# Kernel tuning notes

Hardware: AMD Instinct MI355X
Metric: run time of the kernel (lower is better)

The kernel has to match this reference:

```python
import jax, jax.numpy as jnp
import numpy as np

MAX_EVENTS = 100  # decoder steps (undefined global in source)

def _make_pe(seq_len, d):
    pos = jnp.arange(seq_len, dtype=jnp.float32)[:, None]
    div = jnp.exp(jnp.arange(0, d, 2, dtype=jnp.float32) * (-np.log(10000.0) / d))
    pe = jnp.zeros((seq_len, d), dtype=jnp.float32)
    pe = pe.at[:, 0::2].set(jnp.sin(pos * div))
    pe = pe.at[:, 1::2].set(jnp.cos(pos * div))
    return pe

def _gru_combine(gi, gh, h):
    # PyTorch GRU gate order: r, z, n
    ir, iz, inn = jnp.split(gi, 3, axis=-1)
    hr, hz, hn = jnp.split(gh, 3, axis=-1)
    r = jax.nn.sigmoid(ir + hr)
    z = jax.nn.sigmoid(iz + hz)
    n = jnp.tanh(inn + r * hn)
    return (1.0 - z) * n + z * h

def setup_inputs() -> dict:
    key = jax.random.key(0)
    d = 768
    bs, seq = 64, 300
    ks = jax.random.split(key, 18)
    s = 0.02
    return {
        'x': jax.random.normal(ks[0], (bs, seq, d), jnp.float32),
        'enc_Wih': jax.random.normal(ks[1], (3 * d, d), jnp.float32) * s,
        'enc_Whh': jax.random.normal(ks[2], (3 * d, d), jnp.float32) * s,
        'enc_bih': jax.random.normal(ks[3], (3 * d,), jnp.float32) * s,
        'enc_bhh': jax.random.normal(ks[4], (3 * d,), jnp.float32) * s,
        'dec_Wih': jax.random.normal(ks[5], (3 * d, 1 + d), jnp.float32) * s,
        'dec_Whh': jax.random.normal(ks[6], (3 * d, d), jnp.float32) * s,
        'dec_bih': jax.random.normal(ks[7], (3 * d,), jnp.float32) * s,
        'dec_bhh': jax.random.normal(ks[8], (3 * d,), jnp.float32) * s,
        'qW': jax.random.normal(ks[9], (d, d), jnp.float32) * s,
        'qb': jax.random.normal(ks[10], (d,), jnp.float32) * s,
        'mW': jax.random.normal(ks[11], (d, d), jnp.float32) * s,
        'mb': jax.random.normal(ks[12], (d,), jnp.float32) * s,
        'pW': jax.random.normal(ks[13], (1, d), jnp.float32) * s,
        'pb': jax.random.normal(ks[14], (1,), jnp.float32) * s,
        'tW': jax.random.normal(ks[15], (1, d), jnp.float32) * s,
        'tb': jax.random.normal(ks[16], (1,), jnp.float32) * s,
    }

def reference(x, enc_Wih, enc_Whh, enc_bih, enc_bhh,
              dec_Wih, dec_Whh, dec_bih, dec_bhh,
              qW, qb, mW, mb, pW, pb, tW, tb):
    bs, seq, d = x.shape
    # positional encoding (dropout in eval mode -> identity)
    x = x + _make_pe(seq, d)[None, :, :]

    # encoder GRU: precompute input projections, scan over time
    gi_all = jnp.einsum('bsd,gd->sbg', x, enc_Wih) + enc_bih  # (seq, bs, 3d)
    h0 = jnp.zeros((bs, d), x.dtype)

    def enc_step(h, gi):
        gh = h @ enc_Whh.T + enc_bhh
        h_new = _gru_combine(gi, gh, h)
        return h_new, h_new

    _, enc_seq = jax.lax.scan(enc_step, h0, gi_all)
    enc_outputs = jnp.transpose(enc_seq, (1, 0, 2))  # (bs, seq, d)

    # memory projection (loop-invariant; same math as recomputing each step)
    mem = jnp.einsum('bsd,ed->bse', enc_outputs, mW) + mb  # (bs, seq, d)

    def dec_step(carry, _):
        h, last = carry  # h: (bs, d), last: (bs, 1)
        q = h @ qW.T + qb  # (bs, d)
        logits = jnp.tanh(mem + q[:, None, :]) @ pW[0] + pb[0]  # (bs, seq)
        w = jax.nn.softmax(logits, axis=1)
        ctx = jnp.einsum('bs,bsd->bd', w, enc_outputs)
        xin = jnp.concatenate([last, ctx], axis=-1)  # (bs, 1+d)
        gi = xin @ dec_Wih.T + dec_bih
        gh = h @ dec_Whh.T + dec_bhh
        h_new = _gru_combine(gi, gh, h)
        pred = h_new @ tW.T + tb  # (bs, 1)
        return (h_new, pred), pred

    last0 = jnp.zeros((bs, 1), x.dtype)
    _, preds = jax.lax.scan(dec_step, (h0, last0), None, length=MAX_EVENTS)
    return jnp.transpose(preds, (1, 0, 2))  # (bs, MAX_EVENTS, 1)
```

## Files before the change

### kernel.cpp

```cpp
#include <hip/hip_runtime.h>
#include <hip/hip_bf16.h>
#include <cstdint>
#include <cstddef>

#define D    768
#define G3   2304
#define BS   64
#define SEQ  300
#define TDEC 100
#define TCH  25
#define NCH  12
#define NBLK 512
#define NH   (D * 64)

#define BAR_GRP(g)  ((g) * 32)
#define BAR_TOP     512
#define BAR_GEN0    544
#define BAR_GENL(g) (576 + (g) * 32)
#define BAR_SIZE    2048

typedef unsigned int u32;
typedef unsigned long long u64;

__device__ __forceinline__ float sigf(float x) { return 1.0f / (1.0f + __expf(-x)); }
__device__ __forceinline__ float tanhfast(float x) {
    float e = __expf(2.0f * x);
    return 1.0f - 2.0f / (e + 1.0f);
}
__device__ __forceinline__ void bf2x(u32 u, float& a, float& b) {
    union { u32 i; float f; } xx, yy;
    xx.i = u << 16; yy.i = u & 0xffff0000u; a = xx.f; b = yy.f;
}

#define DOT4(acc, wv, x0, x1, x2, x3) \
    acc = fmaf((wv).x,(x0), fmaf((wv).y,(x1), fmaf((wv).z,(x2), fmaf((wv).w,(x3),(acc)))))

__device__ __forceinline__ void stG(float* p, float v) {
    __hip_atomic_store(p, v, __ATOMIC_RELAXED, __HIP_MEMORY_SCOPE_AGENT);
}
__device__ __forceinline__ void stG64(u64* p, u64 v) {
    __hip_atomic_store(p, v, __ATOMIC_RELAXED, __HIP_MEMORY_SCOPE_AGENT);
}
__device__ __forceinline__ float ldGf(const float* p) {
    return __hip_atomic_load(p, __ATOMIC_RELAXED, __HIP_MEMORY_SCOPE_AGENT);
}
__device__ __forceinline__ u32 ldGu(const u32* p) {
    return __hip_atomic_load(p, __ATOMIC_RELAXED, __HIP_MEMORY_SCOPE_AGENT);
}
__device__ __forceinline__ u32 f2bfu(float f) {
    __hip_bfloat16 h = __float2bfloat16(f);
    unsigned short s; __builtin_memcpy(&s, &h, 2); return (u32)s;
}
__device__ __forceinline__ float bfsel(u32 w, int sh) {
    union { u32 i; float f; } u; u.i = ((w >> sh) & 0xffffu) << 16; return u.f;
}

__device__ __forceinline__ void gridbar(u32* B, u32 idx) {
    __builtin_amdgcn_fence(__ATOMIC_RELEASE, "workgroup");
    __syncthreads();
    if (threadIdx.x == 0) {
        const u32 g = blockIdx.x >> 5;
        u32 old = __hip_atomic_fetch_add(&B[BAR_GRP(g)], 1u, __ATOMIC_RELAXED, __HIP_MEMORY_SCOPE_AGENT);
        if (old == idx * 32u - 1u) {
            u32 o2 = __hip_atomic_fetch_add(&B[BAR_TOP], 1u, __ATOMIC_RELAXED, __HIP_MEMORY_SCOPE_AGENT);
            if (o2 == idx * 16u - 1u) {
                __hip_atomic_store(&B[BAR_GEN0], idx, __ATOMIC_RELAXED, __HIP_MEMORY_SCOPE_AGENT);
            } else {
                while (__hip_atomic_load(&B[BAR_GEN0], __ATOMIC_RELAXED, __HIP_MEMORY_SCOPE_AGENT) < idx)
                    __builtin_amdgcn_s_sleep(4);
            }
            __hip_atomic_store(&B[BAR_GENL(g)], idx, __ATOMIC_RELAXED, __HIP_MEMORY_SCOPE_AGENT);
        } else {
            while (__hip_atomic_load(&B[BAR_GENL(g)], __ATOMIC_RELAXED, __HIP_MEMORY_SCOPE_AGENT) < idx)
                __builtin_amdgcn_s_sleep(8);
        }
    }
    __syncthreads();
}

__global__ __launch_bounds__(256) void kPrep(
    const float* __restrict__ decWih,
    float* __restrict__ Wc, float* __restrict__ W0,
    float* __restrict__ hSeq0, float* __restrict__ hDs0,
    float* __restrict__ lastP, u32* __restrict__ barW)
{
    const int NW = G3 * 769;
    const int NB = 2 * BAR_SIZE;
    const int TOT = NW + 2 * NH + 64 + NB;
    const int stride = gridDim.x * blockDim.x;
    for (int u = blockIdx.x * blockDim.x + threadIdx.x; u < TOT; u += stride) {
        if (u < NW) {
            int g = u / 769; int c = u % 769;
            float w = decWih[u];
            if (c == 0) W0[g] = w; else Wc[(size_t)g * D + (c - 1)] = w;
        } else if (u < NW + NH) {
            hSeq0[u - NW] = 0.0f;
        } else if (u < NW + 2 * NH) {
            hDs0[u - NW - NH] = 0.0f;
        } else if (u < NW + 2 * NH + 64) {
            lastP[u - NW - 2 * NH] = 0.0f;
        } else {
            barW[u - NW - 2 * NH - 64] = 0;
        }
    }
}

__device__ __forceinline__ void gi_tile(
    const float* __restrict__ x, const float* __restrict__ Wih,
    __hip_bfloat16* __restrict__ giB, float* __restrict__ As, float* __restrict__ Bs,
    int m0, int tc, int t)
{
    const int tid = threadIdx.x;
    const int lr = tid >> 2;
    const int lk = (tid & 3) * 4;
    const int tm = (tid >> 4) * 4;
    const int tn = (tid & 15) * 4;
    const float tf = (float)t;

    float acc[4][4];
    #pragma unroll
    for (int i = 0; i < 4; ++i)
        #pragma unroll
        for (int j = 0; j < 4; ++j) acc[i][j] = 0.f;

    for (int kc = 0; kc < D; kc += 16) {
        const float4 a4 = *(const float4*)(Wih + (size_t)(m0 + lr) * D + kc + lk);
        float4 b4 = *(const float4*)(x + ((size_t)lr * SEQ + t) * D + kc + lk);
        const int i0 = (kc + lk) >> 1;
        const float dv0 = __expf(-0.0239852614f * (float)i0);
        const float dv1 = __expf(-0.0239852614f * (float)(i0 + 1));
        float s0, c0, s1, c1;
        __sincosf(tf * dv0, &s0, &c0);
        __sincosf(tf * dv1, &s1, &c1);
        b4.x += s0; b4.y += c0; b4.z += s1; b4.w += c1;
        As[(lk + 0) * 64 + lr] = a4.x; As[(lk + 1) * 64 + lr] = a4.y;
        As[(lk + 2) * 64 + lr] = a4.z; As[(lk + 3) * 64 + lr] = a4.w;
        Bs[(lk + 0) * 64 + lr] = b4.x; Bs[(lk + 1) * 64 + lr] = b4.y;
        Bs[(lk + 2) * 64 + lr] = b4.z; Bs[(lk + 3) * 64 + lr] = b4.w;
        __syncthreads();
        #pragma unroll
        for (int k = 0; k < 16; ++k) {
            const float4 av = *(const float4*)(As + k * 64 + tm);
            const float4 bv = *(const float4*)(Bs + k * 64 + tn);
            acc[0][0] = fmaf(av.x, bv.x, acc[0][0]); acc[0][1] = fmaf(av.x, bv.y, acc[0][1]);
            acc[0][2] = fmaf(av.x, bv.z, acc[0][2]); acc[0][3] = fmaf(av.x, bv.w, acc[0][3]);
            acc[1][0] = fmaf(av.y, bv.x, acc[1][0]); acc[1][1] = fmaf(av.y, bv.y, acc[1][1]);
            acc[1][2] = fmaf(av.y, bv.z, acc[1][2]); acc[1][3] = fmaf(av.y, bv.w, acc[1][3]);
            acc[2][0] = fmaf(av.z, bv.x, acc[2][0]); acc[2][1] = fmaf(av.z, bv.y, acc[2][1]);
            acc[2][2] = fmaf(av.z, bv.z, acc[2][2]); acc[2][3] = fmaf(av.z, bv.w, acc[2][3]);
            acc[3][0] = fmaf(av.w, bv.x, acc[3][0]); acc[3][1] = fmaf(av.w, bv.y, acc[3][1]);
            acc[3][2] = fmaf(av.w, bv.z, acc[3][2]); acc[3][3] = fmaf(av.w, bv.w, acc[3][3]);
        }
        __syncthreads();
    }
    #pragma unroll
    for (int i = 0; i < 4; ++i) {
        u32 lo = f2bfu(acc[i][0]) | (f2bfu(acc[i][1]) << 16);
        u32 hi = f2bfu(acc[i][2]) | (f2bfu(acc[i][3]) << 16);
        u64 v = ((u64)hi << 32) | (u64)lo;
        stG64((u64*)(giB + ((size_t)tc * G3 + m0 + tm + i) * 64 + tn), v);
    }
}

__device__ __forceinline__ void enc_step(
    const __hip_bfloat16* __restrict__ giT, const float* __restrict__ Whh,
    const float* __restrict__ bih, const float* __restrict__ bhh,
    const float* __restrict__ hrd, float* __restrict__ hwr,
    __hip_bfloat16* __restrict__ encB, int t, float* __restrict__ lds_h)
{
    const int tid = threadIdx.x;
    const int b   = tid & 63;
    const int jw  = __builtin_amdgcn_readfirstlane((int)(blockIdx.x * 4 + (tid >> 6)));

    const float* whr = Whh + (size_t)jw * D;
    const float* whz = Whh + (size_t)(768 + jw) * D;
    const float* whn = Whh + (size_t)(1536 + jw) * D;

    float ahr = 0.f, ahz = 0.f, ahn = 0.f;
    for (int kc = 0; kc < D; kc += 64) {
        const float4* gh = (const float4*)(hrd + kc * 64);
        float4* lh = (float4*)lds_h;
        #pragma unroll
        for (int it = 0; it < 4; ++it) lh[tid + 256 * it] = gh[tid + 256 * it];
        __syncthreads();
        #pragma unroll
        for (int kk = 0; kk < 64; kk += 4) {
            const float4 v3 = *(const float4*)(whr + kc + kk);
            const float4 v4 = *(const float4*)(whz + kc + kk);
            const float4 v5 = *(const float4*)(whn + kc + kk);
            const float h0 = lds_h[(kk + 0) * 64 + b];
            const float h1 = lds_h[(kk + 1) * 64 + b];
            const float h2 = lds_h[(kk + 2) * 64 + b];
            const float h3 = lds_h[(kk + 3) * 64 + b];
            DOT4(ahr, v3, h0, h1, h2, h3);
            DOT4(ahz, v4, h0, h1, h2, h3);
            DOT4(ahn, v5, h0, h1, h2, h3);
        }
        __syncthreads();
    }
    const u32* gp = (const u32*)giT;
    const int bo = b >> 1, sh = (b & 1) << 4;
    const u32 w0 = ldGu(gp + (size_t)jw * 32 + bo);
    const u32 w1 = ldGu(gp + (size_t)(768 + jw) * 32 + bo);
    const u32 w2 = ldGu(gp + (size_t)(1536 + jw) * 32 + bo);
    const float gir = bfsel(w0, sh);
    const float giz = bfsel(w1, sh);
    const float gin = bfsel(w2, sh);
    const float r = sigf(gir + bih[jw] + ahr + bhh[jw]);
    const float z = sigf(giz + bih[768 + jw] + ahz + bhh[768 + jw]);
    const float n = tanhfast(gin + bih[1536 + jw] + r * (ahn + bhh[1536 + jw]));
    const float ho = hrd[jw * 64 + b];
    const float hn = (1.f - z) * n + z * ho;
    stG(hwr + jw * 64 + b, hn);
    encB[((size_t)b * SEQ + t) * D + jw] = __float2bfloat16(hn);
}

__global__ __launch_bounds__(256) void kEncPersist(
    const float* __restrict__ x, const float* __restrict__ eWih,
    const float* __restrict__ eWhh, const float* __restrict__ ebih,
    const float* __restrict__ ebhh, __hip_bfloat16* __restrict__ giB,
    float* __restrict__ hSeq, __hip_bfloat16* __restrict__ encB, u32* bar)
{
    __shared__ float smem[4096];
    u32 bars = 0;
    for (int c = 0; c < NCH; ++c) {
        for (int job = blockIdx.x; job < 36 * TCH; job += NBLK)
            gi_tile(x, eWih, giB, smem, smem + 1024,
                    (job % 36) * 64, job / 36, c * TCH + job / 36);
        gridbar(bar, ++bars);
        for (int tc = 0; tc < TCH; ++tc) {
            const int t = c * TCH + tc;
            if (blockIdx.x < 192)
                enc_step(giB + (size_t)tc * G3 * 64, eWhh, ebih, ebhh,
                         hSeq + (size_t)t * NH, hSeq + (size_t)(t + 1) * NH, encB, t, smem);
            gridbar(bar, ++bars);
        }
    }
}

__global__ __launch_bounds__(256) void kGemmMem(
    const __hip_bfloat16* __restrict__ encB, const float* __restrict__ mW,
    const float* __restrict__ mb, __hip_bfloat16* __restrict__ memB)
{
    __shared__ float As[16 * 64];
    __shared__ float Bs[16 * 64];
    const int tid = threadIdx.x;
    const int m0 = blockIdx.y * 64, n0 = blockIdx.x * 64;
    const int lr = tid >> 2;
    const int lk = (tid & 3) * 4;
    const int tm = (tid >> 4) * 4;
    const int tn = (tid & 15) * 4;

    float acc[4][4];
    #pragma unroll
    for (int i = 0; i < 4; ++i)
        #pragma unroll
        for (int j = 0; j < 4; ++j) acc[i][j] = 0.f;

    for (int kc = 0; kc < D; kc += 16) {
        const uint2 ua = *(const uint2*)(encB + (size_t)(m0 + lr) * D + kc + lk);
        float a0, a1, a2, a3;
        bf2x(ua.x, a0, a1); bf2x(ua.y, a2, a3);
        const float4 b4 = *(const float4*)(mW + (size_t)(n0 + lr) * D + kc + lk);
        As[(lk + 0) * 64 + lr] = a0; As[(lk + 1) * 64 + lr] = a1;
        As[(lk + 2) * 64 + lr] = a2; As[(lk + 3) * 64 + lr] = a3;
        Bs[(lk + 0) * 64 + lr] = b4.x; Bs[(lk + 1) * 64 + lr] = b4.y;
        Bs[(lk + 2) * 64 + lr] = b4.z; Bs[(lk + 3) * 64 + lr] = b4.w;
        __syncthreads();
        #pragma unroll
        for (int k = 0; k < 16; ++k) {
            const float4 av = *(const float4*)(As + k * 64 + tm);
            const float4 bv = *(const float4*)(Bs + k * 64 + tn);
            acc[0][0] = fmaf(av.x, bv.x, acc[0][0]); acc[0][1] = fmaf(av.x, bv.y, acc[0][1]);
            acc[0][2] = fmaf(av.x, bv.z, acc[0][2]); acc[0][3] = fmaf(av.x, bv.w, acc[0][3]);
            acc[1][0] = fmaf(av.y, bv.x, acc[1][0]); acc[1][1] = fmaf(av.y, bv.y, acc[1][1]);
            acc[1][2] = fmaf(av.y, bv.z, acc[1][2]); acc[1][3] = fmaf(av.y, bv.w, acc[1][3]);
            acc[2][0] = fmaf(av.z, bv.x, acc[2][0]); acc[2][1] = fmaf(av.z, bv.y, acc[2][1]);
            acc[2][2] = fmaf(av.z, bv.z, acc[2][2]); acc[2][3] = fmaf(av.z, bv.w, acc[2][3]);
            acc[3][0] = fmaf(av.w, bv.x, acc[3][0]); acc[3][1] = fmaf(av.w, bv.y, acc[3][1]);
            acc[3][2] = fmaf(av.w, bv.z, acc[3][2]); acc[3][3] = fmaf(av.w, bv.w, acc[3][3]);
        }
        __syncthreads();
    }
    const float bb0 = mb[n0 + tn + 0], bb1 = mb[n0 + tn + 1];
    const float bb2 = mb[n0 + tn + 2], bb3 = mb[n0 + tn + 3];
    #pragma unroll
    for (int i = 0; i < 4; ++i) {
        __hip_bfloat16* row = memB + (size_t)(m0 + tm + i) * D + n0 + tn;
        row[0] = __float2bfloat16(acc[i][0] + bb0);
        row[1] = __float2bfloat16(acc[i][1] + bb1);
        row[2] = __float2bfloat16(acc[i][2] + bb2);
        row[3] = __float2bfloat16(acc[i][3] + bb3);
    }
}

__device__ __forceinline__ void dec_q(
    const float* __restrict__ qW, const float* __restrict__ qb,
    const float* __restrict__ hrd, float* __restrict__ qTt,
    float* __restrict__ lds_h, float* __restrict__ lds_t)
{
    const int tid = threadIdx.x;
    const int b   = tid & 63;
    const int wv  = tid >> 6;
    const int jw  = __builtin_amdgcn_readfirstlane((int)(blockIdx.x * 4 + wv));
    const float* w = qW + (size_t)jw * D;
    float acc = 0.f;
    for (int kc = 0; kc < D; kc += 64) {
        const float4* gh = (const float4*)(hrd + kc * 64);
        float4* lh = (float4*)lds_h;
        #pragma unroll
        for (int it = 0; it < 4; ++it) lh[tid + 256 * it] = gh[tid + 256 * it];
        __syncthreads();
        #pragma unroll
        for (int kk = 0; kk < 64; kk += 4) {
            const float4 w4 = *(const float4*)(w + kc + kk);
            acc = fmaf(w4.x, lds_h[(kk + 0) * 64 + b], acc);
            acc = fmaf(w4.y, lds_h[(kk + 1) * 64 + b], acc);
            acc = fmaf(w4.z, lds_h[(kk + 2) * 64 + b], acc);
            acc = fmaf(w4.w, lds_h[(kk + 3) * 64 + b], acc);
        }
        __syncthreads();
    }
    lds_t[b * 4 + wv] = acc + qb[jw];
    __syncthreads();
    if (tid < 128) {
        const int bb = tid >> 1, hf = (tid & 1) * 2;
        float2 v; v.x = lds_t[bb * 4 + hf]; v.y = lds_t[bb * 4 + hf + 1];
        u64 uv; __builtin_memcpy(&uv, &v, 8);
        stG64((u64*)(qTt + (size_t)bb * D + blockIdx.x * 4 + hf), uv);
    }
}

__device__ __forceinline__ void dec_attn(
    const float* __restrict__ qTt, const __hip_bfloat16* __restrict__ memB,
    const __hip_bfloat16* __restrict__ encB, const float* __restrict__ pW,
    const float* __restrict__ pb, float* __restrict__ ctxP, float* __restrict__ seP,
    float* __restrict__ sm)
{
    const int tid = threadIdx.x;
    const int b  = blockIdx.x & 63;
    const int ch = blockIdx.x >> 6;
    float* s_q  = sm;
    float* s_pw = sm + 768;
    float* s_cx = sm + 1536;
    float* s_se = sm + 2304;
    for (int i = tid; i < 768; i += 256) {
        s_q[i]  = qTt[(size_t)b * D + i];
        s_pw[i] = pW[i];
        s_cx[i] = 0.f;
    }
    if (tid == 0) s_se[0] = 0.f;
    __syncthreads();
    const int lane = tid & 63;
    const int wv   = tid >> 6;
    const int d0_0 = lane * 4, d0_1 = 256 + lane * 4, d0_2 = 512 + lane * 4;
    const float4 qv0 = *(const float4*)(s_q + d0_0);
    const float4 qv1 = *(const float4*)(s_q + d0_1);
    const float4 qv2 = *(const float4*)(s_q + d0_2);
    const float4 pv0 = *(const float4*)(s_pw + d0_0);
    const float4 pv1 = *(const float4*)(s_pw + d0_1);
    const float4 pv2 = *(const float4*)(s_pw + d0_2);
    float cacc[12];
    #pragma unroll
    for (int i = 0; i < 12; ++i) cacc[i] = 0.f;
    float seacc = 0.f;
    const float pbv = pb[0];
    const size_t rowb = (size_t)b * SEQ;
    int s = ch + 8 * wv;
    uint2 mu0, mu1, mu2, eu0, eu1, eu2;
    if (s < SEQ) {
        const __hip_bfloat16* mrow = memB + (rowb + s) * D;
        const __hip_bfloat16* erow = encB + (rowb + s) * D;
        mu0 = *(const uint2*)(mrow + d0_0); mu1 = *(const uint2*)(mrow + d0_1); mu2 = *(const uint2*)(mrow + d0_2);
        eu0 = *(const uint2*)(erow + d0_0); eu1 = *(const uint2*)(erow + d0_1); eu2 = *(const uint2*)(erow + d0_2);
    }
    while (s < SEQ) {
        const int sn = s + 32;
        const bool pf = sn < SEQ;
        uint2 nm0, nm1, nm2, ne0, ne1, ne2;
        if (pf) {
            const __hip_bfloat16* mrow = memB + (rowb + sn) * D;
            const __hip_bfloat16* erow = encB + (rowb + sn) * D;
            nm0 = *(const uint2*)(mrow + d0_0); nm1 = *(const uint2*)(mrow + d0_1); nm2 = *(const uint2*)(mrow + d0_2);
            ne0 = *(const uint2*)(erow + d0_0); ne1 = *(const uint2*)(erow + d0_1); ne2 = *(const uint2*)(erow + d0_2);
        }
        float lp = 0.f;
        float m0, m1, m2, m3;
        bf2x(mu0.x, m0, m1); bf2x(mu0.y, m2, m3);
        lp = fmaf(pv0.x, tanhfast(m0 + qv0.x), lp);
        lp = fmaf(pv0.y, tanhfast(m1 + qv0.y), lp);
        lp = fmaf(pv0.z, tanhfast(m2 + qv0.z), lp);
        lp = fmaf(pv0.w, tanhfast(m3 + qv0.w), lp);
        bf2x(mu1.x, m0, m1); bf2x(mu1.y, m2, m3);
        lp = fmaf(pv1.x, tanhfast(m0 + qv1.x), lp);
        lp = fmaf(pv1.y, tanhfast(m1 + qv1.y), lp);
        lp = fmaf(pv1.z, tanhfast(m2 + qv1.z), lp);
        lp = fmaf(pv1.w, tanhfast(m3 + qv1.w), lp);
        bf2x(mu2.x, m0, m1); bf2x(mu2.y, m2, m3);
        lp = fmaf(pv2.x, tanhfast(m0 + qv2.x), lp);
        lp = fmaf(pv2.y, tanhfast(m1 + qv2.y), lp);
        lp = fmaf(pv2.z, tanhfast(m2 + qv2.z), lp);
        lp = fmaf(pv2.w, tanhfast(m3 + qv2.w), lp);
        #pragma unroll
        for (int o = 32; o > 0; o >>= 1) lp += __shfl_xor(lp, o, 64);
        const float e = __expf(lp + pbv);
        seacc += e;
        float e0, e1, e2, e3;
        bf2x(eu0.x, e0, e1); bf2x(eu0.y, e2, e3);
        cacc[0] = fmaf(e, e0, cacc[0]); cacc[1] = fmaf(e, e1, cacc[1]);
        cacc[2] = fmaf(e, e2, cacc[2]); cacc[3] = fmaf(e, e3, cacc[3]);
        bf2x(eu1.x, e0, e1); bf2x(eu1.y, e2, e3);
        cacc[4] = fmaf(e, e0, cacc[4]); cacc[5] = fmaf(e, e1, cacc[5]);
        cacc[6] = fmaf(e, e2, cacc[6]); cacc[7] = fmaf(e, e3, cacc[7]);
        bf2x(eu2.x, e0, e1); bf2x(eu2.y, e2, e3);
        cacc[8]  = fmaf(e, e0, cacc[8]);  cacc[9]  = fmaf(e, e1, cacc[9]);
        cacc[10] = fmaf(e, e2, cacc[10]); cacc[11] = fmaf(e, e3, cacc[11]);
        if (pf) { mu0 = nm0; mu1 = nm1; mu2 = nm2; eu0 = ne0; eu1 = ne1; eu2 = ne2; }
        s = sn;
    }
    #pragma unroll
    for (int g = 0; g < 3; ++g) {
        const int d0 = g * 256 + lane * 4;
        atomicAdd(&s_cx[d0 + 0], cacc[g * 4 + 0]);
        atomicAdd(&s_cx[d0 + 1], cacc[g * 4 + 1]);
        atomicAdd(&s_cx[d0 + 2], cacc[g * 4 + 2]);
        atomicAdd(&s_cx[d0 + 3], cacc[g * 4 + 3]);
    }
    if (lane == 0) atomicAdd(&s_se[0], seacc);
    __syncthreads();
    float* crow = ctxP + (size_t)(ch * 64 + b) * D;
    for (int i = tid; i < 768; i += 256) stG(crow + i, s_cx[i]);
    if (tid == 0) stG(seP + ch * 64 + b, s_se[0]);
}

__device__ __forceinline__ void dec_combine(
    const float* __restrict__ ctxP, const float* __restrict__ seP,
    float* __restrict__ ctxCt, float* __restrict__ seCt)
{
    const int b = blockIdx.x;
    const int tid = threadIdx.x;
    for (int i = tid; i < 768; i += 256) {
        float s = 0.f;
        #pragma unroll
        for (int ch = 0; ch < 8; ++ch)
            s += ldGf(ctxP + (size_t)(ch * 64 + b) * D + i);
        stG(ctxCt + (size_t)b * D + i, s);
    }
    if (tid == 0) {
        float s = 0.f;
        #pragma unroll
        for (int ch = 0; ch < 8; ++ch) s += ldGf(seP + ch * 64 + b);
        stG(seCt + b, s);
    }
}

__device__ __forceinline__ void dec_reduce(
    const float* __restrict__ ppt, const float* __restrict__ tb,
    float* __restrict__ lastN, float* __restrict__ out, int t, float* __restrict__ sm)
{
    const int b = blockIdx.x - 448;
    const int tid = threadIdx.x;
    float v = 0.f;
    if (tid < 192) v = ppt[(size_t)b * 192 + tid];
    #pragma unroll
    for (int o = 32; o > 0; o >>= 1) v += __shfl_xor(v, o, 64);
    if ((tid & 63) == 0) sm[tid >> 6] = v;
    __syncthreads();
    if (tid == 0) {
        const float p = sm[0] + sm[1] + sm[2] + sm[3] + tb[0];
        out[(size_t)b * TDEC + t] = p;
        stG(lastN + b, p);
    }
    __syncthreads();
}

__device__ __forceinline__ void dec_cell(
    const float* __restrict__ Wc, const float* __restrict__ W0,
    const float* __restrict__ dWhh, const float* __restrict__ dbih,
    const float* __restrict__ dbhh, const float* __restrict__ tW,
    const float* __restrict__ ctxFt, const float* __restrict__ seFt,
    const float* __restrict__ lastT, float* __restrict__ ppt,
    const float* __restrict__ hrd, float* __restrict__ hwr,
    float* __restrict__ lds_h, float* __restrict__ lds_c)
{
    const int tid = threadIdx.x;
    const int b   = tid & 63;
    const int q4  = tid >> 6;
    const int jw  = __builtin_amdgcn_readfirstlane((int)(blockIdx.x * 4 + q4));
    const float* whr = dWhh + (size_t)jw * D;
    const float* whz = dWhh + (size_t)(768 + jw) * D;
    const float* whn = dWhh + (size_t)(1536 + jw) * D;
    const float* wcr = Wc + (size_t)jw * D;
    const float* wcz = Wc + (size_t)(768 + jw) * D;
    const float* wcn = Wc + (size_t)(1536 + jw) * D;
    float cir = 0.f, ciz = 0.f, cin_ = 0.f, ahr = 0.f, ahz = 0.f, ahn = 0.f;
    for (int kc = 0; kc < D; kc += 64) {
        const float4* gh = (const float4*)(hrd + kc * 64);
        float4* lh = (float4*)lds_h;
        #pragma unroll
        for (int it = 0; it < 4; ++it) lh[tid + 256 * it] = gh[tid + 256 * it];
        {
            const float4* cp = (const float4*)(ctxFt + (size_t)b * D + kc + q4 * 16);
            const float4 c0 = cp[0], c1 = cp[1], c2 = cp[2], c3 = cp[3];
            const int k0 = q4 * 16;
            lds_c[(k0 +  0) * 64 + b] = c0.x; lds_c[(k0 +  1) * 64 + b] = c0.y;
            lds_c[(k0 +  2) * 64 + b] = c0.z; lds_c[(k0 +  3) * 64 + b] = c0.w;
            lds_c[(k0 +  4) * 64 + b] = c1.x; lds_c[(k0 +  5) * 64 + b] = c1.y;
            lds_c[(k0 +  6) * 64 + b] = c1.z; lds_c[(k0 +  7) * 64 + b] = c1.w;
            lds_c[(k0 +  8) * 64 + b] = c2.x; lds_c[(k0 +  9) * 64 + b] = c2.y;
            lds_c[(k0 + 10) * 64 + b] = c2.z; lds_c[(k0 + 11) * 64 + b] = c2.w;
            lds_c[(k0 + 12) * 64 + b] = c3.x; lds_c[(k0 + 13) * 64 + b] = c3.y;
            lds_c[(k0 + 14) * 64 + b] = c3.z; lds_c[(k0 + 15) * 64 + b] = c3.w;
        }
        __syncthreads();
        #pragma unroll
        for (int kk = 0; kk < 64; kk += 4) {
            const float4 v0 = *(const float4*)(wcr + kc + kk);
            const float4 v1 = *(const float4*)(wcz + kc + kk);
            const float4 v2 = *(const float4*)(wcn + kc + kk);
            const float4 v3 = *(const float4*)(whr + kc + kk);
            const float4 v4 = *(const float4*)(whz + kc + kk);
            const float4 v5 = *(const float4*)(whn + kc + kk);
            const float c0 = lds_c[(kk + 0) * 64 + b];
            const float c1 = lds_c[(kk + 1) * 64 + b];
            const float c2 = lds_c[(kk + 2) * 64 + b];
            const float c3 = lds_c[(kk + 3) * 64 + b];
            const float h0 = lds_h[(kk + 0) * 64 + b];
            const float h1 = lds_h[(kk + 1) * 64 + b];
            const float h2 = lds_h[(kk + 2) * 64 + b];
            const float h3 = lds_h[(kk + 3) * 64 + b];
            DOT4(cir, v0, c0, c1, c2, c3);
            DOT4(ciz, v1, c0, c1, c2, c3);
            DOT4(cin_, v2, c0, c1, c2, c3);
            DOT4(ahr, v3, h0, h1, h2, h3);
            DOT4(ahz, v4, h0, h1, h2, h3);
            DOT4(ahn, v5, h0, h1, h2, h3);
        }
        __syncthreads();
    }
    const float inv = 1.f / seFt[b];
    const float lst = lastT[b];
    const float gir = cir * inv + W0[jw] * lst + dbih[jw];
    const float giz = ciz * inv + W0[768 + jw] * lst + dbih[768 + jw];
    const float gin = cin_ * inv + W0[1536 + jw] * lst + dbih[1536 + jw];
    const float r = sigf(gir + ahr + dbhh[jw]);
    const float z = sigf(giz + ahz + dbhh[768 + jw]);
    const float n = tanhfast(gin + r * (ahn + dbhh[1536 + jw]));
    const float ho = hrd[jw * 64 + b];
    const float hn = (1.f - z) * n + z * ho;
    stG(hwr + jw * 64 + b, hn);

    __syncthreads();
    lds_h[q4 * 64 + b] = tW[jw] * hn;
    __syncthreads();
    if (tid < 64) {
        const float p = lds_h[tid] + lds_h[64 + tid] + lds_h[128 + tid] + lds_h[192 + tid];
        stG(ppt + (size_t)tid * 192 + blockIdx.x, p);
    }
}

__global__ __launch_bounds__(256) void kDecPersist(
    const float* __restrict__ Wc, const float* __restrict__ W0,
    const float* __restrict__ dWhh, const float* __restrict__ dbih,
    const float* __restrict__ dbhh, const float* __restrict__ tW,
    const float* __restrict__ tb, const float* __restrict__ qW,
    const float* __restrict__ qb,
    const __hip_bfloat16* __restrict__ memB, const __hip_bfloat16* __restrict__ encB,
    const float* __restrict__ pW, const float* __restrict__ pb,
    float* __restrict__ qTu, float* __restrict__ ctxP, float* __restrict__ seP,
    float* __restrict__ ctxC, float* __restrict__ seC,
    float* __restrict__ predP, float* __restrict__ lastP,
    float* __restrict__ hDs, float* __restrict__ out, u32* bar)
{
    __shared__ float smem[8192];
    u32 bars = 0;
    for (int t = 0; t < TDEC; ++t) {
        const float* hr = hDs + (size_t)t * NH;
        float*       hw = hDs + (size_t)(t + 1) * NH;
        if (blockIdx.x < 192)
            dec_q(qW, qb, hr, qTu + (size_t)t * BS * D, smem, smem + 4096);
        else if (blockIdx.x >= 448 && t > 0)
            dec_reduce(predP + (size_t)(t - 1) * 64 * 192, tb,
                       lastP + (size_t)t * 64, out, t - 1, smem);
        gridbar(bar, ++bars);
        dec_attn(qTu + (size_t)t * BS * D, memB, encB, pW, pb, ctxP, seP, smem);
        gridbar(bar, ++bars);
        if (blockIdx.x < 64)
            dec_combine(ctxP, seP, ctxC + (size_t)t * BS * D, seC + (size_t)t * 64);
        gridbar(bar, ++bars);
        if (blockIdx.x < 192)
            dec_cell(Wc, W0, dWhh, dbih, dbhh, tW,
                     ctxC + (size_t)t * BS * D, seC + (size_t)t * 64,
                     lastP + (size_t)t * 64, predP + (size_t)t * 64 * 192,
                     hr, hw, smem, smem + 4096);
        gridbar(bar, ++bars);
    }
    if (blockIdx.x >= 448)
        dec_reduce(predP + (size_t)(TDEC - 1) * 64 * 192, tb,
                   lastP + (size_t)TDEC * 64, out, TDEC - 1, smem);
}

extern "C" void kernel_launch(void* const* d_in, const int* in_sizes, int n_in,
                              void* d_out, int out_size, void* d_ws, size_t ws_size,
                              hipStream_t stream) {
    const float* x    = (const float*)d_in[0];
    const float* eWih = (const float*)d_in[1];
    const float* eWhh = (const float*)d_in[2];
    const float* ebih = (const float*)d_in[3];
    const float* ebhh = (const float*)d_in[4];
    const float* dWih = (const float*)d_in[5];
    const float* dWhh = (const float*)d_in[6];
    const float* dbih = (const float*)d_in[7];
    const float* dbhh = (const float*)d_in[8];
    const float* qW   = (const float*)d_in[9];
    const float* qb   = (const float*)d_in[10];
    const float* mW   = (const float*)d_in[11];
    const float* mb   = (const float*)d_in[12];
    const float* pW   = (const float*)d_in[13];
    const float* pb   = (const float*)d_in[14];
    const float* tW   = (const float*)d_in[15];
    const float* tb   = (const float*)d_in[16];
    float* out = (float*)d_out;

    char* w = (char*)d_ws;
    auto alloc = [&](size_t bytes) -> char* {
        char* p = w; w += (bytes + 255) & ~(size_t)255; return p;
    };
    float* Wc    = (float*)alloc((size_t)G3 * D * 4);
    float* W0    = (float*)alloc((size_t)G3 * 4);
    __hip_bfloat16* encB = (__hip_bfloat16*)alloc((size_t)BS * SEQ * D * 2);
    __hip_bfloat16* memB = (__hip_bfloat16*)alloc((size_t)BS * SEQ * D * 2);
    __hip_bfloat16* giB  = (__hip_bfloat16*)alloc((size_t)TCH * G3 * 64 * 2);
    float* hSeq  = (float*)alloc((size_t)(SEQ + 1) * NH * 4);
    float* hDs   = (float*)alloc((size_t)(TDEC + 1) * NH * 4);
    float* qTu   = (float*)alloc((size_t)TDEC * BS * D * 4);
    float* ctxP  = (float*)alloc((size_t)8 * BS * D * 4);
    float* seP   = (float*)alloc(8 * 64 * 4);
    float* ctxC  = (float*)alloc((size_t)TDEC * BS * D * 4);
    float* seC   = (float*)alloc((size_t)TDEC * 64 * 4);
    float* predP = (float*)alloc((size_t)TDEC * 64 * 192 * 4);
    float* lastP = (float*)alloc((size_t)(TDEC + 1) * 64 * 4);
    u32*   barW  = (u32*)alloc((size_t)2 * BAR_SIZE * 4);

    kPrep<<<512, 256, 0, stream>>>(dWih, Wc, W0, hSeq, hDs, lastP, barW);
    kEncPersist<<<NBLK, 256, 0, stream>>>(x, eWih, eWhh, ebih, ebhh, giB, hSeq, encB, barW);
    kGemmMem<<<dim3(12, 300), 256, 0, stream>>>(encB, mW, mb, memB);
    kDecPersist<<<NBLK, 256, 0, stream>>>(Wc, W0, dWhh, dbih, dbhh, tW, tb, qW, qb,
                                          memB, encB, pW, pb, qTu, ctxP, seP, ctxC, seC,
                                          predP, lastP, hDs, out, barW + BAR_SIZE);
}
```

Baseline: 23.30 ms.

## Add XCD-local fast grid barriers and overlap encoder input GEMM with recurrence

New measurement: 22.26 ms. 4.4% less time.

```diff
diff --git a/kernel.cpp b/kernel.cpp
--- a/kernel.cpp
+++ b/kernel.cpp
@@ -13,11 +13,21 @@
 #define NBLK 512
 #define NH   (D * 64)
 
-#define BAR_GRP(g)  ((g) * 32)
-#define BAR_TOP     512
-#define BAR_GEN0    544
-#define BAR_GENL(g) (576 + (g) * 32)
-#define BAR_SIZE    2048
+#define R_SLOW_GRP(g)  ((g) * 32)
+#define R_SLOW_TOP     512
+#define R_SLOW_GEN0    544
+#define R_SLOW_GENL(g) (576 + (g) * 32)
+#define R_FA_LARR      1088
+#define R_FA_GENL      1344
+#define R_FA_TOP       1600
+#define R_FA_GEN0      1632
+#define R_FB_LARR      1664
+#define R_FB_GENL      1920
+#define R_FB_TOP       2176
+#define R_FB_GEN0      2208
+#define R_PROBE(g)     (2240 + (g) * 32)
+#define R_VOTE         2496
+#define R_SIZE         4096
 
 typedef unsigned int u32;
 typedef unsigned long long u64;
@@ -55,27 +65,80 @@
     union { u32 i; float f; } u; u.i = ((w >> sh) & 0xffffu) << 16; return u.f;
 }
 
-__device__ __forceinline__ void gridbar(u32* B, u32 idx) {
+__device__ __forceinline__ u32 add_wg(u32* p, u32 v) {
+    return __hip_atomic_fetch_add(p, v, __ATOMIC_RELAXED, __HIP_MEMORY_SCOPE_WORKGROUP);
+}
+__device__ __forceinline__ u32 add_ag(u32* p, u32 v) {
+    return __hip_atomic_fetch_add(p, v, __ATOMIC_RELAXED, __HIP_MEMORY_SCOPE_AGENT);
+}
+__device__ __forceinline__ void st_ag(u32* p, u32 v) {
+    __hip_atomic_store(p, v, __ATOMIC_RELAXED, __HIP_MEMORY_SCOPE_AGENT);
+}
+__device__ __forceinline__ u32 ld_ag(const u32* p) {
+    return __hip_atomic_load(p, __ATOMIC_RELAXED, __HIP_MEMORY_SCOPE_AGENT);
+}
+
+__device__ __forceinline__ uint2 ldnt2(const __hip_bfloat16* p) {
+    u64 v = __builtin_nontemporal_load((const u64*)p);
+    uint2 r; r.x = (u32)v; r.y = (u32)(v >> 32); return r;
+}
+
+__device__ __forceinline__ void bar_slow(u32* B, u32 idx) {
     __builtin_amdgcn_fence(__ATOMIC_RELEASE, "workgroup");
     __syncthreads();
     if (threadIdx.x == 0) {
         const u32 g = blockIdx.x >> 5;
-        u32 old = __hip_atomic_fetch_add(&B[BAR_GRP(g)], 1u, __ATOMIC_RELAXED, __HIP_MEMORY_SCOPE_AGENT);
+        u32 old = add_ag(&B[R_SLOW_GRP(g)], 1u);
         if (old == idx * 32u - 1u) {
-            u32 o2 = __hip_atomic_fetch_add(&B[BAR_TOP], 1u, __ATOMIC_RELAXED, __HIP_MEMORY_SCOPE_AGENT);
+            u32 o2 = add_ag(&B[R_SLOW_TOP], 1u);
             if (o2 == idx * 16u - 1u) {
-                __hip_atomic_store(&B[BAR_GEN0], idx, __ATOMIC_RELAXED, __HIP_MEMORY_SCOPE_AGENT);
+                st_ag(&B[R_SLOW_GEN0], idx);
             } else {
-                while (__hip_atomic_load(&B[BAR_GEN0], __ATOMIC_RELAXED, __HIP_MEMORY_SCOPE_AGENT) < idx)
-                    __builtin_amdgcn_s_sleep(4);
+                while (ld_ag(&B[R_SLOW_GEN0]) < idx) __builtin_amdgcn_s_sleep(4);
             }
-            __hip_atomic_store(&B[BAR_GENL(g)], idx, __ATOMIC_RELAXED, __HIP_MEMORY_SCOPE_AGENT);
+            st_ag(&B[R_SLOW_GENL(g)], idx);
         } else {
-            while (__hip_atomic_load(&B[BAR_GENL(g)], __ATOMIC_RELAXED, __HIP_MEMORY_SCOPE_AGENT) < idx)
-                __builtin_amdgcn_s_sleep(8);
-        }
-    }
-    __syncthreads();
+            while (ld_ag(&B[R_SLOW_GENL(g)]) < idx) __builtin_amdgcn_s_sleep(8);
+        }
+    }
+    __syncthreads();
+}
+
+__device__ __forceinline__ void bar_fast(u32* R, int larr, int genl, int top, int gen0,
+                                         u32 idx, u32 perClass) {
+    __builtin_amdgcn_fence(__ATOMIC_RELEASE, "workgroup");
+    __syncthreads();
+    if (threadIdx.x == 0) {
+        const int g = blockIdx.x & 7;
+        u32 old = add_wg(&R[larr + g * 32], 1u);
+        if (old == idx * perClass - 1u) {
+            u32 o2 = add_ag(&R[top], 1u);
+            if (o2 == idx * 8u - 1u) {
+                st_ag(&R[gen0], idx);
+            } else {
+                while (ld_ag(&R[gen0]) < idx) __builtin_amdgcn_s_sleep(2);
+            }
+            st_ag(&R[genl + g * 32], idx);
+        } else {
+            while (ld_ag(&R[genl + g * 32]) < idx) __builtin_amdgcn_s_sleep(4);
+        }
+    }
+    __syncthreads();
+}
+#define BAR_FA(R, i, n) bar_fast((R), R_FA_LARR, R_FA_GENL, R_FA_TOP, R_FA_GEN0, (i), (n))
+#define BAR_FB(R, i, n) bar_fast((R), R_FB_LARR, R_FB_GENL, R_FB_TOP, R_FB_GEN0, (i), (n))
+
+__device__ __forceinline__ u32 censusRun(u32* R, u32* sflag) {
+    if (threadIdx.x == 0) add_wg(&R[R_PROBE(blockIdx.x & 7)], 1u);
+    bar_slow(R, 1);
+    if (threadIdx.x == 0) {
+        u32 old = add_wg(&R[R_PROBE(blockIdx.x & 7)], 1u);
+        add_ag(&R[R_VOTE], (old >= (u32)(NBLK / 8)) ? 1u : 0u);
+    }
+    bar_slow(R, 2);
+    if (threadIdx.x == 0) *sflag = (ld_ag(&R[R_VOTE]) == (u32)NBLK) ? 1u : 0u;
+    __syncthreads();
+    return *sflag;
 }
 
 __global__ __launch_bounds__(256) void kPrep(
@@ -85,7 +148,7 @@
     float* __restrict__ lastP, u32* __restrict__ barW)
 {
     const int NW = G3 * 769;
-    const int NB = 2 * BAR_SIZE;
+    const int NB = 2 * R_SIZE;
     const int TOT = NW + 2 * NH + 64 + NB;
     const int stride = gridDim.x * blockDim.x;
     for (int u = blockIdx.x * blockDim.x + threadIdx.x; u < TOT; u += stride) {
@@ -219,21 +282,50 @@
     const float* __restrict__ x, const float* __restrict__ eWih,
     const float* __restrict__ eWhh, const float* __restrict__ ebih,
     const float* __restrict__ ebhh, __hip_bfloat16* __restrict__ giB,
-    float* __restrict__ hSeq, __hip_bfloat16* __restrict__ encB, u32* bar)
+    float* __restrict__ hSeq, __hip_bfloat16* __restrict__ encB, u32* R)
 {
     __shared__ float smem[4096];
-    u32 bars = 0;
+    __shared__ u32 sflag;
+    const u32 fast = censusRun(R, &sflag);
+    const int bid = blockIdx.x;
+    const size_t GSZ = (size_t)TCH * G3 * 64;
+    u32 si = 2, fE = 0, fS = 0;
+
+    for (int job = bid; job < 36 * TCH; job += NBLK)
+        gi_tile(x, eWih, giB, smem, smem + 1024, (job % 36) * 64, job / 36, job / 36);
+    if (fast) BAR_FA(R, ++fE, 64); else bar_slow(R, ++si);
+
     for (int c = 0; c < NCH; ++c) {
-        for (int job = blockIdx.x; job < 36 * TCH; job += NBLK)
-            gi_tile(x, eWih, giB, smem, smem + 1024,
-                    (job % 36) * 64, job / 36, c * TCH + job / 36);
-        gridbar(bar, ++bars);
-        for (int tc = 0; tc < TCH; ++tc) {
-            const int t = c * TCH + tc;
-            if (blockIdx.x < 192)
-                enc_step(giB + (size_t)tc * G3 * 64, eWhh, ebih, ebhh,
-                         hSeq + (size_t)t * NH, hSeq + (size_t)(t + 1) * NH, encB, t, smem);
-            gridbar(bar, ++bars);
+        __hip_bfloat16* gcur = giB + (size_t)(c & 1) * GSZ;
+        __hip_bfloat16* gnxt = giB + (size_t)((c + 1) & 1) * GSZ;
+        if (fast) {
+            if (bid < 192) {
+                for (int tc = 0; tc < TCH; ++tc) {
+                    const int t = c * TCH + tc;
+                    enc_step(gcur + (size_t)tc * G3 * 64, eWhh, ebih, ebhh,
+                             hSeq + (size_t)t * NH, hSeq + (size_t)(t + 1) * NH, encB, t, smem);
+                    BAR_FB(R, ++fS, 24);
+                }
+            } else if (c + 1 < NCH) {
+                for (int j = bid - 192; j < 36 * TCH; j += 320)
+                    gi_tile(x, eWih, gnxt, smem, smem + 1024,
+                            (j % 36) * 64, j / 36, (c + 1) * TCH + j / 36);
+            }
+            BAR_FA(R, ++fE, 64);
+        } else {
+            for (int tc = 0; tc < TCH; ++tc) {
+                const int t = c * TCH + tc;
+                if (bid < 192)
+                    enc_step(gcur + (size_t)tc * G3 * 64, eWhh, ebih, ebhh,
+                             hSeq + (size_t)t * NH, hSeq + (size_t)(t + 1) * NH, encB, t, smem);
+                bar_slow(R, ++si);
+            }
+            if (c + 1 < NCH) {
+                for (int job = bid; job < 36 * TCH; job += NBLK)
+                    gi_tile(x, eWih, gnxt, smem, smem + 1024,
+                            (job % 36) * 64, job / 36, (c + 1) * TCH + job / 36);
+                bar_slow(R, ++si);
+            }
         }
     }
 }
@@ -371,8 +463,8 @@
     if (s < SEQ) {
         const __hip_bfloat16* mrow = memB + (rowb + s) * D;
         const __hip_bfloat16* erow = encB + (rowb + s) * D;
-        mu0 = *(const uint2*)(mrow + d0_0); mu1 = *(const uint2*)(mrow + d0_1); mu2 = *(const uint2*)(mrow + d0_2);
-        eu0 = *(const uint2*)(erow + d0_0); eu1 = *(const uint2*)(erow + d0_1); eu2 = *(const uint2*)(erow + d0_2);
+        mu0 = ldnt2(mrow + d0_0); mu1 = ldnt2(mrow + d0_1); mu2 = ldnt2(mrow + d0_2);
+        eu0 = ldnt2(erow + d0_0); eu1 = ldnt2(erow + d0_1); eu2 = ldnt2(erow + d0_2);
     }
     while (s < SEQ) {
         const int sn = s + 32;
@@ -381,8 +473,8 @@
         if (pf) {
             const __hip_bfloat16* mrow = memB + (rowb + sn) * D;
             const __hip_bfloat16* erow = encB + (rowb + sn) * D;
-            nm0 = *(const uint2*)(mrow + d0_0); nm1 = *(const uint2*)(mrow + d0_1); nm2 = *(const uint2*)(mrow + d0_2);
-            ne0 = *(const uint2*)(erow + d0_0); ne1 = *(const uint2*)(erow + d0_1); ne2 = *(const uint2*)(erow + d0_2);
+            nm0 = ldnt2(mrow + d0_0); nm1 = ldnt2(mrow + d0_1); nm2 = ldnt2(mrow + d0_2);
+            ne0 = ldnt2(erow + d0_0); ne1 = ldnt2(erow + d0_1); ne2 = ldnt2(erow + d0_2);
         }
         float lp = 0.f;
         float m0, m1, m2, m3;
@@ -570,10 +662,12 @@
     float* __restrict__ qTu, float* __restrict__ ctxP, float* __restrict__ seP,
     float* __restrict__ ctxC, float* __restrict__ seC,
     float* __restrict__ predP, float* __restrict__ lastP,
-    float* __restrict__ hDs, float* __restrict__ out, u32* bar)
+    float* __restrict__ hDs, float* __restrict__ out, u32* R)
 {
     __shared__ float smem[8192];
-    u32 bars = 0;
+    __shared__ u32 sflag;
+    const u32 fast = censusRun(R, &sflag);
+    u32 si = 2, fA = 0;
     for (int t = 0; t < TDEC; ++t) {
         const float* hr = hDs + (size_t)t * NH;
         float*       hw = hDs + (size_t)(t + 1) * NH;
@@ -582,18 +676,18 @@
         else if (blockIdx.x >= 448 && t > 0)
             dec_reduce(predP + (size_t)(t - 1) * 64 * 192, tb,
                        lastP + (size_t)t * 64, out, t - 1, smem);
-        gridbar(bar, ++bars);
+        if (fast) BAR_FA(R, ++fA, 64); else bar_slow(R, ++si);
         dec_attn(qTu + (size_t)t * BS * D, memB, encB, pW, pb, ctxP, seP, smem);
-        gridbar(bar, ++bars);
+        if (fast) BAR_FA(R, ++fA, 64); else bar_slow(R, ++si);
         if (blockIdx.x < 64)
             dec_combine(ctxP, seP, ctxC + (size_t)t * BS * D, seC + (size_t)t * 64);
-        gridbar(bar, ++bars);
+        if (fast) BAR_FA(R, ++fA, 64); else bar_slow(R, ++si);
         if (blockIdx.x < 192)
             dec_cell(Wc, W0, dWhh, dbih, dbhh, tW,
                      ctxC + (size_t)t * BS * D, seC + (size_t)t * 64,
                      lastP + (size_t)t * 64, predP + (size_t)t * 64 * 192,
                      hr, hw, smem, smem + 4096);
-        gridbar(bar, ++bars);
+        if (fast) BAR_FA(R, ++fA, 64); else bar_slow(R, ++si);
     }
     if (blockIdx.x >= 448)
         dec_reduce(predP + (size_t)(TDEC - 1) * 64 * 192, tb,
@@ -630,7 +724,7 @@
     float* W0    = (float*)alloc((size_t)G3 * 4);
     __hip_bfloat16* encB = (__hip_bfloat16*)alloc((size_t)BS * SEQ * D * 2);
     __hip_bfloat16* memB = (__hip_bfloat16*)alloc((size_t)BS * SEQ * D * 2);
-    __hip_bfloat16* giB  = (__hip_bfloat16*)alloc((size_t)TCH * G3 * 64 * 2);
+    __hip_bfloat16* giB  = (__hip_bfloat16*)alloc((size_t)2 * TCH * G3 * 64 * 2);
     float* hSeq  = (float*)alloc((size_t)(SEQ + 1) * NH * 4);
     float* hDs   = (float*)alloc((size_t)(TDEC + 1) * NH * 4);
     float* qTu   = (float*)alloc((size_t)TDEC * BS * D * 4);
@@ -640,12 +734,12 @@
     float* seC   = (float*)alloc((size_t)TDEC * 64 * 4);
     float* predP = (float*)alloc((size_t)TDEC * 64 * 192 * 4);
     float* lastP = (float*)alloc((size_t)(TDEC + 1) * 64 * 4);
-    u32*   barW  = (u32*)alloc((size_t)2 * BAR_SIZE * 4);
+    u32*   barW  = (u32*)alloc((size_t)2 * R_SIZE * 4);
 
     kPrep<<<512, 256, 0, stream>>>(dWih, Wc, W0, hSeq, hDs, lastP, barW);
     kEncPersist<<<NBLK, 256, 0, stream>>>(x, eWih, eWhh, ebih, ebhh, giB, hSeq, encB, barW);
     kGemmMem<<<dim3(12, 300), 256, 0, stream>>>(encB, mW, mb, memB);
     kDecPersist<<<NBLK, 256, 0, stream>>>(Wc, W0, dWhh, dbih, dbhh, tW, tb, qW, qb,
                                           memB, encB, pW, pb, qTu, ctxP, seP, ctxC, seC,
-                                          predP, lastP, hDs, out, barW + BAR_SIZE);
-}
+                                          predP, lastP, hDs, out, barW + R_SIZE);
+}
```

## Overlap encoder input projection with recurrence and use flag-array grid barriers

Applied to the files above, without the earlier changes.

New measurement: 23.22 ms. No clear change (-0.3%).

```diff
diff --git a/kernel.cpp b/kernel.cpp
--- a/kernel.cpp
+++ b/kernel.cpp
@@ -13,11 +13,7 @@
 #define NBLK 512
 #define NH   (D * 64)
 
-#define BAR_GRP(g)  ((g) * 32)
-#define BAR_TOP     512
-#define BAR_GEN0    544
-#define BAR_GENL(g) (576 + (g) * 32)
-#define BAR_SIZE    2048
+#define BAR_WORDS 2048
 
 typedef unsigned int u32;
 typedef unsigned long long u64;
@@ -47,6 +43,12 @@
 __device__ __forceinline__ u32 ldGu(const u32* p) {
     return __hip_atomic_load(p, __ATOMIC_RELAXED, __HIP_MEMORY_SCOPE_AGENT);
 }
+__device__ __forceinline__ void st_ag(u32* p, u32 v) {
+    __hip_atomic_store(p, v, __ATOMIC_RELAXED, __HIP_MEMORY_SCOPE_AGENT);
+}
+__device__ __forceinline__ u32 ld_ag(const u32* p) {
+    return __hip_atomic_load(p, __ATOMIC_RELAXED, __HIP_MEMORY_SCOPE_AGENT);
+}
 __device__ __forceinline__ u32 f2bfu(float f) {
     __hip_bfloat16 h = __float2bfloat16(f);
     unsigned short s; __builtin_memcpy(&s, &h, 2); return (u32)s;
@@ -55,26 +57,26 @@
     union { u32 i; float f; } u; u.i = ((w >> sh) & 0xffffu) << 16; return u.f;
 }
 
-__device__ __forceinline__ void gridbar(u32* B, u32 idx) {
+__device__ __forceinline__ uint2 ldnt2(const __hip_bfloat16* p) {
+    u64 v = __builtin_nontemporal_load((const u64*)p);
+    uint2 r; r.x = (u32)v; r.y = (u32)(v >> 32); return r;
+}
+
+__device__ __forceinline__ void bar_all(u32* F, u32 idx) {
     __builtin_amdgcn_fence(__ATOMIC_RELEASE, "workgroup");
     __syncthreads();
-    if (threadIdx.x == 0) {
-        const u32 g = blockIdx.x >> 5;
-        u32 old = __hip_atomic_fetch_add(&B[BAR_GRP(g)], 1u, __ATOMIC_RELAXED, __HIP_MEMORY_SCOPE_AGENT);
-        if (old == idx * 32u - 1u) {
-            u32 o2 = __hip_atomic_fetch_add(&B[BAR_TOP], 1u, __ATOMIC_RELAXED, __HIP_MEMORY_SCOPE_AGENT);
-            if (o2 == idx * 16u - 1u) {
-                __hip_atomic_store(&B[BAR_GEN0], idx, __ATOMIC_RELAXED, __HIP_MEMORY_SCOPE_AGENT);
-            } else {
-                while (__hip_atomic_load(&B[BAR_GEN0], __ATOMIC_RELAXED, __HIP_MEMORY_SCOPE_AGENT) < idx)
-                    __builtin_amdgcn_s_sleep(4);
-            }
-            __hip_atomic_store(&B[BAR_GENL(g)], idx, __ATOMIC_RELAXED, __HIP_MEMORY_SCOPE_AGENT);
-        } else {
-            while (__hip_atomic_load(&B[BAR_GENL(g)], __ATOMIC_RELAXED, __HIP_MEMORY_SCOPE_AGENT) < idx)
-                __builtin_amdgcn_s_sleep(8);
-        }
-    }
+    const int tid = threadIdx.x;
+    if (tid == 0) st_ag(&F[blockIdx.x], idx);
+    while (ld_ag(&F[tid]) < idx) __builtin_amdgcn_s_sleep(8);
+    while (ld_ag(&F[tid + 256]) < idx) __builtin_amdgcn_s_sleep(8);
+    __syncthreads();
+}
+__device__ __forceinline__ void bar_192(u32* F, u32 idx) {
+    __builtin_amdgcn_fence(__ATOMIC_RELEASE, "workgroup");
+    __syncthreads();
+    const int tid = threadIdx.x;
+    if (tid == 0) st_ag(&F[blockIdx.x], idx);
+    if (tid < 192) { while (ld_ag(&F[tid]) < idx) __builtin_amdgcn_s_sleep(8); }
     __syncthreads();
 }
 
@@ -85,8 +87,7 @@
     float* __restrict__ lastP, u32* __restrict__ barW)
 {
     const int NW = G3 * 769;
-    const int NB = 2 * BAR_SIZE;
-    const int TOT = NW + 2 * NH + 64 + NB;
+    const int TOT = NW + 2 * NH + 64 + BAR_WORDS;
     const int stride = gridDim.x * blockDim.x;
     for (int u = blockIdx.x * blockDim.x + threadIdx.x; u < TOT; u += stride) {
         if (u < NW) {
@@ -219,22 +220,34 @@
     const float* __restrict__ x, const float* __restrict__ eWih,
     const float* __restrict__ eWhh, const float* __restrict__ ebih,
     const float* __restrict__ ebhh, __hip_bfloat16* __restrict__ giB,
-    float* __restrict__ hSeq, __hip_bfloat16* __restrict__ encB, u32* bar)
+    float* __restrict__ hSeq, __hip_bfloat16* __restrict__ encB,
+    u32* EF, u32* EN)
 {
     __shared__ float smem[4096];
-    u32 bars = 0;
+    const int bid = blockIdx.x;
+    const size_t GSZ = (size_t)TCH * G3 * 64;
+    u32 fe = 0, fn = 0;
+
+    for (int job = bid; job < 36 * TCH; job += NBLK)
+        gi_tile(x, eWih, giB, smem, smem + 1024, (job % 36) * 64, job / 36, job / 36);
+    bar_all(EF, ++fe);
+
     for (int c = 0; c < NCH; ++c) {
-        for (int job = blockIdx.x; job < 36 * TCH; job += NBLK)
-            gi_tile(x, eWih, giB, smem, smem + 1024,
-                    (job % 36) * 64, job / 36, c * TCH + job / 36);
-        gridbar(bar, ++bars);
-        for (int tc = 0; tc < TCH; ++tc) {
-            const int t = c * TCH + tc;
-            if (blockIdx.x < 192)
-                enc_step(giB + (size_t)tc * G3 * 64, eWhh, ebih, ebhh,
+        __hip_bfloat16* gcur = giB + (size_t)(c & 1) * GSZ;
+        __hip_bfloat16* gnxt = giB + (size_t)((c + 1) & 1) * GSZ;
+        if (bid < 192) {
+            for (int tc = 0; tc < TCH; ++tc) {
+                const int t = c * TCH + tc;
+                enc_step(gcur + (size_t)tc * G3 * 64, eWhh, ebih, ebhh,
                          hSeq + (size_t)t * NH, hSeq + (size_t)(t + 1) * NH, encB, t, smem);
-            gridbar(bar, ++bars);
-        }
+                bar_192(EN, ++fn);
+            }
+        } else if (c + 1 < NCH) {
+            for (int j = bid - 192; j < 36 * TCH; j += 320)
+                gi_tile(x, eWih, gnxt, smem, smem + 1024,
+                        (j % 36) * 64, j / 36, (c + 1) * TCH + j / 36);
+        }
+        bar_all(EF, ++fe);
     }
 }
 
@@ -371,8 +384,8 @@
     if (s < SEQ) {
         const __hip_bfloat16* mrow = memB + (rowb + s) * D;
         const __hip_bfloat16* erow = encB + (rowb + s) * D;
-        mu0 = *(const uint2*)(mrow + d0_0); mu1 = *(const uint2*)(mrow + d0_1); mu2 = *(const uint2*)(mrow + d0_2);
-        eu0 = *(const uint2*)(erow + d0_0); eu1 = *(const uint2*)(erow + d0_1); eu2 = *(const uint2*)(erow + d0_2);
+        mu0 = ldnt2(mrow + d0_0); mu1 = ldnt2(mrow + d0_1); mu2 = ldnt2(mrow + d0_2);
+        eu0 = ldnt2(erow + d0_0); eu1 = ldnt2(erow + d0_1); eu2 = ldnt2(erow + d0_2);
     }
     while (s < SEQ) {
         const int sn = s + 32;
@@ -381,8 +394,8 @@
         if (pf) {
             const __hip_bfloat16* mrow = memB + (rowb + sn) * D;
             const __hip_bfloat16* erow = encB + (rowb + sn) * D;
-            nm0 = *(const uint2*)(mrow + d0_0); nm1 = *(const uint2*)(mrow + d0_1); nm2 = *(const uint2*)(mrow + d0_2);
-            ne0 = *(const uint2*)(erow + d0_0); ne1 = *(const uint2*)(erow + d0_1); ne2 = *(const uint2*)(erow + d0_2);
+            nm0 = ldnt2(mrow + d0_0); nm1 = ldnt2(mrow + d0_1); nm2 = ldnt2(mrow + d0_2);
+            ne0 = ldnt2(erow + d0_0); ne1 = ldnt2(erow + d0_1); ne2 = ldnt2(erow + d0_2);
         }
         float lp = 0.f;
         float m0, m1, m2, m3;
@@ -570,10 +583,10 @@
     float* __restrict__ qTu, float* __restrict__ ctxP, float* __restrict__ seP,
     float* __restrict__ ctxC, float* __restrict__ seC,
     float* __restrict__ predP, float* __restrict__ lastP,
-    float* __restrict__ hDs, float* __restrict__ out, u32* bar)
+    float* __restrict__ hDs, float* __restrict__ out, u32* DF)
 {
     __shared__ float smem[8192];
-    u32 bars = 0;
+    u32 fi = 0;
     for (int t = 0; t < TDEC; ++t) {
         const float* hr = hDs + (size_t)t * NH;
         float*       hw = hDs + (size_t)(t + 1) * NH;
@@ -582,18 +595,18 @@
         else if (blockIdx.x >= 448 && t > 0)
             dec_reduce(predP + (size_t)(t - 1) * 64 * 192, tb,
                        lastP + (size_t)t * 64, out, t - 1, smem);
-        gridbar(bar, ++bars);
+        bar_all(DF, ++fi);
         dec_attn(qTu + (size_t)t * BS * D, memB, encB, pW, pb, ctxP, seP, smem);
-        gridbar(bar, ++bars);
+        bar_all(DF, ++fi);
         if (blockIdx.x < 64)
             dec_combine(ctxP, seP, ctxC + (size_t)t * BS * D, seC + (size_t)t * 64);
-        gridbar(bar, ++bars);
+        bar_all(DF, ++fi);
         if (blockIdx.x < 192)
             dec_cell(Wc, W0, dWhh, dbih, dbhh, tW,
                      ctxC + (size_t)t * BS * D, seC + (size_t)t * 64,
                      lastP + (size_t)t * 64, predP + (size_t)t * 64 * 192,
                      hr, hw, smem, smem + 4096);
-        gridbar(bar, ++bars);
+        bar_all(DF, ++fi);
     }
     if (blockIdx.x >= 448)
         dec_reduce(predP + (size_t)(TDEC - 1) * 64 * 192, tb,
@@ -630,7 +643,7 @@
     float* W0    = (float*)alloc((size_t)G3 * 4);
     __hip_bfloat16* encB = (__hip_bfloat16*)alloc((size_t)BS * SEQ * D * 2);
     __hip_bfloat16* memB = (__hip_bfloat16*)alloc((size_t)BS * SEQ * D * 2);
-    __hip_bfloat16* giB  = (__hip_bfloat16*)alloc((size_t)TCH * G3 * 64 * 2);
+    __hip_bfloat16* giB  = (__hip_bfloat16*)alloc((size_t)2 * TCH * G3 * 64 * 2);
     float* hSeq  = (float*)alloc((size_t)(SEQ + 1) * NH * 4);
     float* hDs   = (float*)alloc((size_t)(TDEC + 1) * NH * 4);
     float* qTu   = (float*)alloc((size_t)TDEC * BS * D * 4);
@@ -640,12 +653,15 @@
     float* seC   = (float*)alloc((size_t)TDEC * 64 * 4);
     float* predP = (float*)alloc((size_t)TDEC * 64 * 192 * 4);
     float* lastP = (float*)alloc((size_t)(TDEC + 1) * 64 * 4);
-    u32*   barW  = (u32*)alloc((size_t)2 * BAR_SIZE * 4);
+    u32*   barW  = (u32*)alloc((size_t)BAR_WORDS * 4);
+    u32*   EF = barW;
+    u32*   EN = barW + 512;
+    u32*   DF = barW + 1024;
 
     kPrep<<<512, 256, 0, stream>>>(dWih, Wc, W0, hSeq, hDs, lastP, barW);
-    kEncPersist<<<NBLK, 256, 0, stream>>>(x, eWih, eWhh, ebih, ebhh, giB, hSeq, encB, barW);
+    kEncPersist<<<NBLK, 256, 0, stream>>>(x, eWih, eWhh, ebih, ebhh, giB, hSeq, encB, EF, EN);
     kGemmMem<<<dim3(12, 300), 256, 0, stream>>>(encB, mW, mb, memB);
     kDecPersist<<<NBLK, 256, 0, stream>>>(Wc, W0, dWhh, dbih, dbhh, tW, tb, qW, qb,
                                           memB, encB, pW, pb, qTu, ctxP, seP, ctxC, seC,
-                                          predP, lastP, hDs, out, barW + BAR_SIZE);
-}
+                                          predP, lastP, hDs, out, DF);
+}
```
